# Performance work log

Hardware: AMD Instinct MI355X
Metric: run time of the kernel (lower is better)

The kernel has to match this reference:

```python
import jax, jax.numpy as jnp
import numpy as np

N_HEADS, DK, DV, G = 12, 64, 64, 1
W_WIN, R_RAND = 3, 2
B, S, D = 2, 2048, 768


def _make_idx_tensor(seq_len, g, w, r, seed=0):
    # Mirrors SparseMultiHeadAttention.create_idx_tensor: each middle row is
    # [0] + r random key indices + w consecutive window key indices.
    rng = np.random.default_rng(seed)
    s2 = seq_len - 2 * g
    shift = max(g - (w - 1) // 2, 0)
    windows = np.arange(s2)[:, None] + np.arange(w)[None, :] + shift  # (s2, w)
    rand = np.empty((s2, r), np.int64)
    half = (w - 1) // 2
    for i in range(s2):
        pos = i + g
        cand = rng.choice(np.arange(1, seq_len), size=r + w + 2, replace=False)
        cand = cand[np.abs(cand - pos) > half][:r]
        rand[i] = cand
    idx = np.concatenate([np.zeros((s2, 1), np.int64), rand, windows], axis=1)
    return jnp.asarray(idx)  # (s2, 1+r+w)


def setup_inputs() -> dict:
    key = jax.random.key(0)
    ks = jax.random.split(key, 7)
    scale = 0.02  # keep projected logits in a sane range for softmax
    return {
        "Q": jax.random.normal(ks[0], (B, S, D), jnp.float32),
        "K": jax.random.normal(ks[1], (B, S, D), jnp.float32),
        "V": jax.random.normal(ks[2], (B, S, D), jnp.float32),
        "Wq": jax.random.normal(ks[3], (N_HEADS * DK, D), jnp.float32) * scale,
        "Wk": jax.random.normal(ks[4], (N_HEADS * DK, D), jnp.float32) * scale,
        "Wv": jax.random.normal(ks[5], (N_HEADS * DV, D), jnp.float32) * scale,
        "Wo": jax.random.normal(ks[6], (D, N_HEADS * DV), jnp.float32) * scale,
        "idx_tensor": _make_idx_tensor(S, G, W_WIN, R_RAND),
    }


def reference(Q, K, V, Wq, Wk, Wv, Wo, idx_tensor):
    b, s, d = Q.shape
    h, dk, dv, g = N_HEADS, DK, DV, G
    # projections (torch Linear: x @ W.T), split heads -> (b, h, s, d_head)
    q = (Q @ Wq.T).reshape(b, s, h, dk).transpose(0, 2, 1, 3)
    k = (K @ Wk.T).reshape(b, s, h, dk).transpose(0, 2, 1, 3)
    v = (V @ Wv.T).reshape(b, s, h, dv).transpose(0, 2, 1, 3)

    # global rows (first g, last g) attend densely over all keys
    gidx = jnp.concatenate([jnp.arange(g), jnp.arange(s - g, s)])
    global_attn = jnp.einsum('bhgd,bhtd->bhgt', q[:, :, gidx, :], k)  # (b,h,2g,s)

    # middle rows: gather [first, random..., window...] keys per row
    comb = k[:, :, idx_tensor, :]                    # (b, h, s2, 1+r+w, dk)
    scores = jnp.einsum('bhsd,bhskd->bhsk', q[:, :, g:s - g, :], comb)

    # scatter into a dense (s, s) score matrix (zeros elsewhere), as the source does
    result = jnp.zeros((b, h, s, s), q.dtype)
    result = result.at[:, :, gidx, :].set(global_attn)
    rows = jnp.arange(g, s - g)[:, None]             # (s2, 1)
    result = result.at[:, :, rows, idx_tensor].set(scores)
    result = result / jnp.sqrt(jnp.asarray(dk, q.dtype))

    attn = jax.nn.softmax(result, axis=-1)
    out = jnp.einsum('bhst,bhtd->bhsd', attn, v)     # (b, h, s, dv)
    out = out.transpose(0, 2, 1, 3).reshape(b, s, h * dv)
    return out @ Wo.T
```

## Files before the change

### kernel.cpp

```cpp
#include <hip/hip_runtime.h>
#include <hip/hip_bf16.h>

#define S_LEN   2048
#define D_MODEL 768
#define NH      12
#define HD      64
#define NI      6
#define S2      2046
#define BB      2
#define NCH     8
#define CHK     256

typedef unsigned short ushort_t;
typedef __attribute__((ext_vector_type(8))) short short8v;
typedef __attribute__((ext_vector_type(4))) float f32x4;

__device__ __forceinline__ unsigned short bf16_rne(float x) {
    union { float f; unsigned int u; } c; c.f = x;
    unsigned int u = c.u + 0x7fffu + ((c.u >> 16) & 1u);
    return (unsigned short)(u >> 16);
}
__device__ __forceinline__ float bf16_f(unsigned short h) {
    union { unsigned int u; float f; } c; c.u = ((unsigned int)h) << 16;
    return c.f;
}

__device__ __forceinline__ void gload16(const ushort_t* g, ushort_t* l) {
    __builtin_amdgcn_global_load_lds(
        (const __attribute__((address_space(1))) void*)g,
        (__attribute__((address_space(3))) void*)l, 16, 0, 0);
}

struct CvtAll {
    const float* Q; const float* K; const float* V;
    const float* Wq; const float* Wk; const float* Wv; const float* Wo;
    ushort_t* Qc; ushort_t* Kc; ushort_t* Vc;
    ushort_t* Wqc; ushort_t* Wkc; ushort_t* Wvc; ushort_t* Woc;
    float* vs;
};

__global__ __launch_bounds__(256) void cvt_all(CvtAll a) {
    const int z = blockIdx.z;
    const int tid = threadIdx.x;
    if (z == 4) {
        if (blockIdx.x == 0)
            for (int i = tid; i < BB * D_MODEL; i += 256) a.vs[i] = 0.f;
        return;
    }
    const float* s; ushort_t* d; long i;
    if (z < 3) {
        s = (z == 0) ? a.Q : (z == 1) ? a.K : a.V;
        d = (z == 0) ? a.Qc : (z == 1) ? a.Kc : a.Vc;
        i = ((long)blockIdx.x * 256 + tid) * 8;
    } else {
        const long WSZ = (long)D_MODEL * D_MODEL;
        long f = ((long)blockIdx.x * 256 + tid) * 8;
        if (f >= 4 * WSZ) return;
        const int which = (int)(f / WSZ);
        i = f % WSZ;
        s = (which == 0) ? a.Wq : (which == 1) ? a.Wk : (which == 2) ? a.Wv : a.Wo;
        d = (which == 0) ? a.Wqc : (which == 1) ? a.Wkc : (which == 2) ? a.Wvc : a.Woc;
    }
    float4 v0 = *(const float4*)&s[i];
    float4 v1 = *(const float4*)&s[i + 4];
    short8v o;
    o[0] = (short)bf16_rne(v0.x); o[1] = (short)bf16_rne(v0.y);
    o[2] = (short)bf16_rne(v0.z); o[3] = (short)bf16_rne(v0.w);
    o[4] = (short)bf16_rne(v1.x); o[5] = (short)bf16_rne(v1.y);
    o[6] = (short)bf16_rne(v1.z); o[7] = (short)bf16_rne(v1.w);
    *(short8v*)&d[i] = o;
}

struct GemmArgs { const ushort_t* A; const ushort_t* W; ushort_t* C; float* Cf; float* vs; };

constexpr int GK = 768, GN = 768, GBK = 32, GNT = GK / GBK;

__global__ __launch_bounds__(256) void bf16_gemm_nt(GemmArgs g0, GemmArgs g1, GemmArgs g2) {
    GemmArgs g = (blockIdx.z == 0) ? g0 : ((blockIdx.z == 1) ? g1 : g2);

    __shared__ ushort_t As[3][4096];
    __shared__ ushort_t Bs[3][4096];

    const int tid  = threadIdx.x;
    const int lane = tid & 63;
    const int w    = tid >> 6;
    const int wm   = w & 1;
    const int wn   = w >> 1;
    const int bm   = blockIdx.y * 128;
    const int bn   = blockIdx.x * 128;
    const int fr   = lane & 15;
    const int blkr = lane >> 4;

    f32x4 acc[4][4];
    #pragma unroll
    for (int i = 0; i < 4; ++i)
        #pragma unroll
        for (int j = 0; j < 4; ++j)
            acc[i][j] = (f32x4){0.f, 0.f, 0.f, 0.f};

    const int row0 = tid >> 2;
    const int row1 = row0 + 64;
    const int blk0 = (tid & 3) ^ ((row0 >> 1) & 3);
    const int blk1 = (tid & 3) ^ ((row1 >> 1) & 3);
    const ushort_t* Ag0 = g.A + (size_t)(bm + row0) * GK + blk0 * 8;
    const ushort_t* Ag1 = g.A + (size_t)(bm + row1) * GK + blk1 * 8;
    const ushort_t* Bg0 = g.W + (size_t)(bn + row0) * GK + blk0 * 8;
    const ushort_t* Bg1 = g.W + (size_t)(bn + row1) * GK + blk1 * 8;
    const int l0 = w * 512;
    const int l1 = 2048 + w * 512;

    int aoff[4], boff[4];
    #pragma unroll
    for (int i = 0; i < 4; ++i) {
        const int ra = wm * 64 + i * 16 + fr;
        aoff[i] = (ra * 4 + (blkr ^ ((ra >> 1) & 3))) * 8;
        const int rb = wn * 64 + i * 16 + fr;
        boff[i] = (rb * 4 + (blkr ^ ((rb >> 1) & 3))) * 8;
    }

    gload16(Ag0, &As[0][l0]); gload16(Ag1, &As[0][l1]);
    gload16(Bg0, &Bs[0][l0]); gload16(Bg1, &Bs[0][l1]);
    gload16(Ag0 + GBK, &As[1][l0]); gload16(Ag1 + GBK, &As[1][l1]);
    gload16(Bg0 + GBK, &Bs[1][l0]); gload16(Bg1 + GBK, &Bs[1][l1]);

    for (int t = 0; t < GNT; ++t) {
        if (t < GNT - 1) asm volatile("s_waitcnt vmcnt(4)" ::: "memory");
        else             asm volatile("s_waitcnt vmcnt(0)" ::: "memory");
        __builtin_amdgcn_s_barrier();

        if (t + 2 < GNT) {
            const int ko = (t + 2) * GBK;
            const int nb = (t + 2) % 3;
            gload16(Ag0 + ko, &As[nb][l0]); gload16(Ag1 + ko, &As[nb][l1]);
            gload16(Bg0 + ko, &Bs[nb][l0]); gload16(Bg1 + ko, &Bs[nb][l1]);
        }

        const ushort_t* as = As[t % 3];
        const ushort_t* bs = Bs[t % 3];
        short8v a[4], b[4];
        #pragma unroll
        for (int i = 0; i < 4; ++i) a[i] = *(const short8v*)&as[aoff[i]];
        #pragma unroll
        for (int i = 0; i < 4; ++i) b[i] = *(const short8v*)&bs[boff[i]];
        #pragma unroll
        for (int i = 0; i < 4; ++i)
            #pragma unroll
            for (int j = 0; j < 4; ++j)
                acc[i][j] = __builtin_amdgcn_mfma_f32_16x16x32_bf16(a[i], b[j], acc[i][j], 0, 0, 0);
    }

    const int crow0 = bm + wm * 64 + ((lane >> 4) << 2);
    const int ccol0 = bn + wn * 64 + fr;
    if (g.Cf) {
        #pragma unroll
        for (int i = 0; i < 4; ++i)
            #pragma unroll
            for (int j = 0; j < 4; ++j)
                #pragma unroll
                for (int r = 0; r < 4; ++r)
                    g.Cf[(size_t)(crow0 + i * 16 + r) * GN + ccol0 + j * 16] = acc[i][j][r];
    } else {
        #pragma unroll
        for (int i = 0; i < 4; ++i)
            #pragma unroll
            for (int j = 0; j < 4; ++j)
                #pragma unroll
                for (int r = 0; r < 4; ++r)
                    g.C[(size_t)(crow0 + i * 16 + r) * GN + ccol0 + j * 16] = bf16_rne(acc[i][j][r]);
        if (g.vs) {
            const int bsel = (bm >= S_LEN) ? 1 : 0;
            #pragma unroll
            for (int j = 0; j < 4; ++j) {
                float part = 0.f;
                #pragma unroll
                for (int i = 0; i < 4; ++i)
                    #pragma unroll
                    for (int r = 0; r < 4; ++r)
                        part += bf16_f(bf16_rne(acc[i][j][r]));
                atomicAdd(&g.vs[bsel * D_MODEL + ccol0 + j * 16], part);
            }
        }
    }
}

__global__ __launch_bounds__(768) void sparse_attn(
    const ushort_t* __restrict__ q, const ushort_t* __restrict__ k, const ushort_t* __restrict__ v,
    const float* __restrict__ vsum, const int* __restrict__ idx,
    ushort_t* __restrict__ ao) {
    const int i0 = blockIdx.x * 2;
    const int b = blockIdx.y;
    const int c = threadIdx.x;

    int id[2][NI];
    #pragma unroll
    for (int r = 0; r < 2; ++r)
        #pragma unroll
        for (int j = 0; j < NI; ++j) id[r][j] = idx[(i0 + r) * NI + j];
    bool dup[2][NI];
    #pragma unroll
    for (int r = 0; r < 2; ++r)
        #pragma unroll
        for (int j = 0; j < NI; ++j) {
            bool d = false;
            #pragma unroll
            for (int j2 = 0; j2 < NI; ++j2)
                if (j2 < j) d = d || (id[r][j2] == id[r][j]);
            dup[r][j] = d;
        }

    const size_t rb0 = ((size_t)(b * S_LEN + i0 + 1)) * D_MODEL + c;
    const float qv0 = bf16_f(q[rb0]);
    const float qv1 = bf16_f(q[rb0 + D_MODEL]);

    float kv[2][NI], vv[2][NI];
    #pragma unroll
    for (int r = 0; r < 2; ++r)
        #pragma unroll
        for (int j = 0; j < NI; ++j) {
            const size_t kb = ((size_t)(b * S_LEN + id[r][j])) * D_MODEL + c;
            kv[r][j] = bf16_f(k[kb]);
            vv[r][j] = bf16_f(v[kb]);
        }

    float p[2][NI];
    #pragma unroll
    for (int j = 0; j < NI; ++j) { p[0][j] = qv0 * kv[0][j]; p[1][j] = qv1 * kv[1][j]; }

    #pragma unroll
    for (int off = 32; off; off >>= 1) {
        #pragma unroll
        for (int r = 0; r < 2; ++r)
            #pragma unroll
            for (int j = 0; j < NI; ++j) p[r][j] += __shfl_xor(p[r][j], off);
    }

    const float vsc = vsum[b * D_MODEL + c];
    #pragma unroll
    for (int r = 0; r < 2; ++r) {
        float acc = vsc;
        float Z = 0.f;
        int u = 0;
        #pragma unroll
        for (int j = 0; j < NI; ++j) {
            if (dup[r][j]) continue;
            float e = expf(p[r][j] * 0.125f);
            Z += e;
            u += 1;
            acc += (e - 1.f) * vv[r][j];
        }
        Z += (float)(S_LEN - u);
        ao[rb0 + (size_t)r * D_MODEL] = bf16_rne(acc / Z);
    }
}

__global__ __launch_bounds__(256) void global_attn_part(
    const ushort_t* __restrict__ q, const ushort_t* __restrict__ k, const ushort_t* __restrict__ v,
    float* __restrict__ part) {
    const int ch = blockIdx.x;
    const int rowsel = blockIdx.y;
    const int row = rowsel ? (S_LEN - 1) : 0;
    const int hb = blockIdx.z;
    const int h = hb % NH;
    const int b = hb / NH;
    const int tid = threadIdx.x;

    __shared__ float qs[HD];
    __shared__ float ps[CHK];
    __shared__ float red[8];
    __shared__ float redv[32][72];

    if (tid < HD) qs[tid] = bf16_f(q[((size_t)(b * S_LEN + row)) * D_MODEL + h * HD + tid]);
    __syncthreads();

    const int t = ch * CHK + tid;
    const ushort_t* kp = &k[((size_t)(b * S_LEN + t)) * D_MODEL + h * HD];
    float s = 0.f;
    #pragma unroll
    for (int dd = 0; dd < 8; ++dd) {
        short8v kk = *(const short8v*)&kp[dd * 8];
        #pragma unroll
        for (int e = 0; e < 8; ++e)
            s += qs[dd * 8 + e] * bf16_f((unsigned short)kk[e]);
    }
    s *= 0.125f;

    float m = s;
    #pragma unroll
    for (int off = 32; off; off >>= 1) m = fmaxf(m, __shfl_xor(m, off));
    if ((tid & 63) == 0) red[tid >> 6] = m;
    __syncthreads();
    m = fmaxf(fmaxf(red[0], red[1]), fmaxf(red[2], red[3]));

    float e = expf(s - m);
    ps[tid] = e;
    float zp = e;
    #pragma unroll
    for (int off = 32; off; off >>= 1) zp += __shfl_xor(zp, off);
    if ((tid & 63) == 0) red[4 + (tid >> 6)] = zp;
    __syncthreads();
    const float E = red[4] + red[5] + red[6] + red[7];

    const int g8 = tid >> 3;
    const int d8 = (tid & 7) * 8;
    float a8[8] = {};
    for (int tt = g8; tt < CHK; tt += 32) {
        const float wgt = ps[tt];
        short8v v8 = *(const short8v*)&v[((size_t)(b * S_LEN + ch * CHK + tt)) * D_MODEL + h * HD + d8];
        #pragma unroll
        for (int e2 = 0; e2 < 8; ++e2)
            a8[e2] += wgt * bf16_f((unsigned short)v8[e2]);
    }
    #pragma unroll
    for (int e2 = 0; e2 < 8; ++e2) redv[g8][d8 + e2] = a8[e2];
    __syncthreads();
    if (tid < HD) {
        float o = 0.f;
        #pragma unroll
        for (int gg = 0; gg < 32; ++gg) o += redv[gg][tid];
        float* pr = part + ((size_t)((hb * 2 + rowsel) * NCH + ch)) * (HD + 2);
        pr[2 + tid] = o;
        if (tid == 0) { pr[0] = m; pr[1] = E; }
    }
}

__global__ __launch_bounds__(64) void global_attn_fin(
    const float* __restrict__ part, ushort_t* __restrict__ ao) {
    const int rb = blockIdx.x;
    const int rowsel = rb & 1;
    const int hb = rb >> 1;
    const int h = hb % NH;
    const int b = hb / NH;
    const int row = rowsel ? (S_LEN - 1) : 0;
    const int d = threadIdx.x;

    const float* pr = part + (size_t)rb * NCH * (HD + 2);
    float M = -1e30f;
    #pragma unroll
    for (int c = 0; c < NCH; ++c) M = fmaxf(M, pr[c * (HD + 2)]);
    float Z = 0.f, acc = 0.f;
    #pragma unroll
    for (int c = 0; c < NCH; ++c) {
        float wgt = expf(pr[c * (HD + 2)] - M);
        Z   += pr[c * (HD + 2) + 1] * wgt;
        acc += pr[c * (HD + 2) + 2 + d] * wgt;
    }
    ao[((size_t)(b * S_LEN + row)) * D_MODEL + h * HD + d] = bf16_rne(acc / Z);
}

extern "C" void kernel_launch(void* const* d_in, const int* in_sizes, int n_in,
                              void* d_out, int out_size, void* d_ws, size_t ws_size,
                              hipStream_t stream) {
    const float* Q  = (const float*)d_in[0];
    const float* K  = (const float*)d_in[1];
    const float* V  = (const float*)d_in[2];
    const float* Wq = (const float*)d_in[3];
    const float* Wk = (const float*)d_in[4];
    const float* Wv = (const float*)d_in[5];
    const float* Wo = (const float*)d_in[6];
    const int*  idx = (const int*)d_in[7];
    float* out = (float*)d_out;

    const size_t SZ  = (size_t)BB * S_LEN * D_MODEL;
    const size_t WSZ = (size_t)D_MODEL * D_MODEL;

    ushort_t* Qc  = (ushort_t*)d_ws;
    ushort_t* Kc  = Qc  + SZ;
    ushort_t* Vc  = Kc  + SZ;
    ushort_t* Wqc = Vc  + SZ;
    ushort_t* Wkc = Wqc + WSZ;
    ushort_t* Wvc = Wkc + WSZ;
    ushort_t* Woc = Wvc + WSZ;
    ushort_t* qb  = Woc + WSZ;
    ushort_t* kb  = qb  + SZ;
    ushort_t* vb  = kb  + SZ;
    ushort_t* ao  = vb  + SZ;
    float* vs   = (float*)(ao + SZ);
    float* part = vs + BB * D_MODEL;

    {
        CvtAll a{Q, K, V, Wq, Wk, Wv, Wo, Qc, Kc, Vc, Wqc, Wkc, Wvc, Woc, vs};
        cvt_all<<<dim3((unsigned)(SZ / 2048), 1, 5), 256, 0, stream>>>(a);
    }
    {
        GemmArgs g0{Qc, Wqc, qb, nullptr, nullptr};
        GemmArgs g1{Kc, Wkc, kb, nullptr, nullptr};
        GemmArgs g2{Vc, Wvc, vb, nullptr, vs};
        bf16_gemm_nt<<<dim3(D_MODEL / 128, BB * S_LEN / 128, 3), 256, 0, stream>>>(g0, g1, g2);
    }
    sparse_attn<<<dim3(S2 / 2, BB), 768, 0, stream>>>(qb, kb, vb, vs, idx, ao);
    global_attn_part<<<dim3(NCH, 2, NH * BB), 256, 0, stream>>>(qb, kb, vb, part);
    global_attn_fin<<<dim3(2 * NH * BB), 64, 0, stream>>>(part, ao);
    {
        GemmArgs g{ao, Woc, nullptr, out, nullptr};
        bf16_gemm_nt<<<dim3(D_MODEL / 128, BB * S_LEN / 128, 1), 256, 0, stream>>>(g, g, g);
    }
}
```

Before: 198.2 us.

## Shrink GEMM M-tile to 64, deepen prefetch to 4 stages, remap workgroups

The bf16 NT GEMM tile shrinks from 128x128 to 64x128, which doubles the workgroup count: 1152 for the QKV projection and 384 for the output projection. This is meant to fill more of the GPU's compute units. The shared-memory pipeline goes from 3 to 4 buffers with a prefetch distance of 3, and the waitcnt thresholds are adjusted to match. Workgroup IDs are remapped with a stride-8 interleave so that neighbouring blocks are spread out across groups. In exchange, each block reuses less data per MFMA and reloads the weight tiles more often.

```diff
diff --git a/kernel.cpp b/kernel.cpp
--- a/kernel.cpp
+++ b/kernel.cpp
@@ -74,86 +74,99 @@
 struct GemmArgs { const ushort_t* A; const ushort_t* W; ushort_t* C; float* Cf; float* vs; };
 
 constexpr int GK = 768, GN = 768, GBK = 32, GNT = GK / GBK;
+constexpr int GX = 6, GY = 64;
 
 __global__ __launch_bounds__(256) void bf16_gemm_nt(GemmArgs g0, GemmArgs g1, GemmArgs g2) {
-    GemmArgs g = (blockIdx.z == 0) ? g0 : ((blockIdx.z == 1) ? g1 : g2);
-
-    __shared__ ushort_t As[3][4096];
-    __shared__ ushort_t Bs[3][4096];
+    const int nwg = GX * GY * gridDim.z;
+    int flat = (blockIdx.z * GY + blockIdx.y) * GX + blockIdx.x;
+    flat = (flat & 7) * (nwg >> 3) + (flat >> 3);
+    const int bz = flat / (GX * GY);
+    const int rem = flat - bz * (GX * GY);
+    const int by = rem / GX;
+    const int bx = rem - by * GX;
+
+    GemmArgs g = (bz == 0) ? g0 : ((bz == 1) ? g1 : g2);
+
+    __shared__ ushort_t As[4][2048];
+    __shared__ ushort_t Bs[4][4096];
 
     const int tid  = threadIdx.x;
     const int lane = tid & 63;
     const int w    = tid >> 6;
     const int wm   = w & 1;
     const int wn   = w >> 1;
-    const int bm   = blockIdx.y * 128;
-    const int bn   = blockIdx.x * 128;
+    const int bm   = by * 64;
+    const int bn   = bx * 128;
     const int fr   = lane & 15;
     const int blkr = lane >> 4;
 
-    f32x4 acc[4][4];
-    #pragma unroll
-    for (int i = 0; i < 4; ++i)
+    f32x4 acc[2][4];
+    #pragma unroll
+    for (int i = 0; i < 2; ++i)
         #pragma unroll
         for (int j = 0; j < 4; ++j)
             acc[i][j] = (f32x4){0.f, 0.f, 0.f, 0.f};
 
     const int row0 = tid >> 2;
-    const int row1 = row0 + 64;
     const int blk0 = (tid & 3) ^ ((row0 >> 1) & 3);
-    const int blk1 = (tid & 3) ^ ((row1 >> 1) & 3);
-    const ushort_t* Ag0 = g.A + (size_t)(bm + row0) * GK + blk0 * 8;
-    const ushort_t* Ag1 = g.A + (size_t)(bm + row1) * GK + blk1 * 8;
+    const ushort_t* Ag  = g.A + (size_t)(bm + row0) * GK + blk0 * 8;
     const ushort_t* Bg0 = g.W + (size_t)(bn + row0) * GK + blk0 * 8;
-    const ushort_t* Bg1 = g.W + (size_t)(bn + row1) * GK + blk1 * 8;
+    const ushort_t* Bg1 = g.W + (size_t)(bn + row0 + 64) * GK + blk0 * 8;
     const int l0 = w * 512;
-    const int l1 = 2048 + w * 512;
-
-    int aoff[4], boff[4];
-    #pragma unroll
-    for (int i = 0; i < 4; ++i) {
-        const int ra = wm * 64 + i * 16 + fr;
+
+    int aoff[2], boff[4];
+    #pragma unroll
+    for (int i = 0; i < 2; ++i) {
+        const int ra = wm * 32 + i * 16 + fr;
         aoff[i] = (ra * 4 + (blkr ^ ((ra >> 1) & 3))) * 8;
-        const int rb = wn * 64 + i * 16 + fr;
-        boff[i] = (rb * 4 + (blkr ^ ((rb >> 1) & 3))) * 8;
-    }
-
-    gload16(Ag0, &As[0][l0]); gload16(Ag1, &As[0][l1]);
-    gload16(Bg0, &Bs[0][l0]); gload16(Bg1, &Bs[0][l1]);
-    gload16(Ag0 + GBK, &As[1][l0]); gload16(Ag1 + GBK, &As[1][l1]);
-    gload16(Bg0 + GBK, &Bs[1][l0]); gload16(Bg1 + GBK, &Bs[1][l1]);
+    }
+    #pragma unroll
+    for (int j = 0; j < 4; ++j) {
+        const int rb = wn * 64 + j * 16 + fr;
+        boff[j] = (rb * 4 + (blkr ^ ((rb >> 1) & 3))) * 8;
+    }
+
+    #pragma unroll
+    for (int t = 0; t < 3; ++t) {
+        const int ko = t * GBK;
+        gload16(Ag + ko, &As[t][l0]);
+        gload16(Bg0 + ko, &Bs[t][l0]);
+        gload16(Bg1 + ko, &Bs[t][2048 + l0]);
+    }
 
     for (int t = 0; t < GNT; ++t) {
-        if (t < GNT - 1) asm volatile("s_waitcnt vmcnt(4)" ::: "memory");
-        else             asm volatile("s_waitcnt vmcnt(0)" ::: "memory");
+        if (t < GNT - 2)      asm volatile("s_waitcnt vmcnt(6)" ::: "memory");
+        else if (t == GNT - 2) asm volatile("s_waitcnt vmcnt(3)" ::: "memory");
+        else                  asm volatile("s_waitcnt vmcnt(0)" ::: "memory");
         __builtin_amdgcn_s_barrier();
 
-        if (t + 2 < GNT) {
-            const int ko = (t + 2) * GBK;
-            const int nb = (t + 2) % 3;
-            gload16(Ag0 + ko, &As[nb][l0]); gload16(Ag1 + ko, &As[nb][l1]);
-            gload16(Bg0 + ko, &Bs[nb][l0]); gload16(Bg1 + ko, &Bs[nb][l1]);
+        if (t + 3 < GNT) {
+            const int ko = (t + 3) * GBK;
+            const int nb = (t + 3) & 3;
+            gload16(Ag + ko, &As[nb][l0]);
+            gload16(Bg0 + ko, &Bs[nb][l0]);
+            gload16(Bg1 + ko, &Bs[nb][2048 + l0]);
         }
 
-        const ushort_t* as = As[t % 3];
-        const ushort_t* bs = Bs[t % 3];
-        short8v a[4], b[4];
-        #pragma unroll
-        for (int i = 0; i < 4; ++i) a[i] = *(const short8v*)&as[aoff[i]];
-        #pragma unroll
-        for (int i = 0; i < 4; ++i) b[i] = *(const short8v*)&bs[boff[i]];
-        #pragma unroll
-        for (int i = 0; i < 4; ++i)
+        const ushort_t* as = As[t & 3];
+        const ushort_t* bs = Bs[t & 3];
+        short8v a[2], b[4];
+        #pragma unroll
+        for (int i = 0; i < 2; ++i) a[i] = *(const short8v*)&as[aoff[i]];
+        #pragma unroll
+        for (int j = 0; j < 4; ++j) b[j] = *(const short8v*)&bs[boff[j]];
+        #pragma unroll
+        for (int i = 0; i < 2; ++i)
             #pragma unroll
             for (int j = 0; j < 4; ++j)
                 acc[i][j] = __builtin_amdgcn_mfma_f32_16x16x32_bf16(a[i], b[j], acc[i][j], 0, 0, 0);
     }
 
-    const int crow0 = bm + wm * 64 + ((lane >> 4) << 2);
+    const int crow0 = bm + wm * 32 + ((lane >> 4) << 2);
     const int ccol0 = bn + wn * 64 + fr;
     if (g.Cf) {
         #pragma unroll
-        for (int i = 0; i < 4; ++i)
+        for (int i = 0; i < 2; ++i)
             #pragma unroll
             for (int j = 0; j < 4; ++j)
                 #pragma unroll
@@ -161,7 +174,7 @@
                     g.Cf[(size_t)(crow0 + i * 16 + r) * GN + ccol0 + j * 16] = acc[i][j][r];
     } else {
         #pragma unroll
-        for (int i = 0; i < 4; ++i)
+        for (int i = 0; i < 2; ++i)
             #pragma unroll
             for (int j = 0; j < 4; ++j)
                 #pragma unroll
@@ -173,7 +186,7 @@
             for (int j = 0; j < 4; ++j) {
                 float part = 0.f;
                 #pragma unroll
-                for (int i = 0; i < 4; ++i)
+                for (int i = 0; i < 2; ++i)
                     #pragma unroll
                     for (int r = 0; r < 4; ++r)
                         part += bf16_f(bf16_rne(acc[i][j][r]));
@@ -385,13 +398,13 @@
         GemmArgs g0{Qc, Wqc, qb, nullptr, nullptr};
         GemmArgs g1{Kc, Wkc, kb, nullptr, nullptr};
         GemmArgs g2{Vc, Wvc, vb, nullptr, vs};
-        bf16_gemm_nt<<<dim3(D_MODEL / 128, BB * S_LEN / 128, 3), 256, 0, stream>>>(g0, g1, g2);
+        bf16_gemm_nt<<<dim3(GX, GY, 3), 256, 0, stream>>>(g0, g1, g2);
     }
     sparse_attn<<<dim3(S2 / 2, BB), 768, 0, stream>>>(qb, kb, vb, vs, idx, ao);
     global_attn_part<<<dim3(NCH, 2, NH * BB), 256, 0, stream>>>(qb, kb, vb, part);
     global_attn_fin<<<dim3(2 * NH * BB), 64, 0, stream>>>(part, ao);
     {
         GemmArgs g{ao, Woc, nullptr, out, nullptr};
-        bf16_gemm_nt<<<dim3(D_MODEL / 128, BB * S_LEN / 128, 1), 256, 0, stream>>>(g, g, g);
-    }
-}
+        bf16_gemm_nt<<<dim3(GX, GY, 1), 256, 0, stream>>>(g, g, g);
+    }
+}
```

Result: slower. 206.3 us (+4.1%).

## Fuse sparse and global attention kernels and remap GEMM workgroups across XCDs

Applied to the files above, without the earlier changes.

Merges the sparse-row attention kernel and the global-row partial attention kernel into one launch, with block ranges dispatched by block index. The global part now runs with 768 threads and spreads its V accumulation over 96 groups. The GEMM also remaps flat workgroup IDs with an XCD-style stride-8 swizzle so neighbouring tiles land on the same chiplet for better L2 reuse. This removes one launch and lets both attention pieces overlap, at the cost of a larger shared-memory footprint per block and more idle threads in the global branch.

```diff
diff --git a/kernel.cpp b/kernel.cpp
--- a/kernel.cpp
+++ b/kernel.cpp
@@ -10,6 +10,7 @@
 #define BB      2
 #define NCH     8
 #define CHK     256
+#define SPB     (S2 / 2)
 
 typedef unsigned short ushort_t;
 typedef __attribute__((ext_vector_type(8))) short short8v;
@@ -74,9 +75,18 @@
 struct GemmArgs { const ushort_t* A; const ushort_t* W; ushort_t* C; float* Cf; float* vs; };
 
 constexpr int GK = 768, GN = 768, GBK = 32, GNT = GK / GBK;
+constexpr int GX = 6, GY = 32;
 
 __global__ __launch_bounds__(256) void bf16_gemm_nt(GemmArgs g0, GemmArgs g1, GemmArgs g2) {
-    GemmArgs g = (blockIdx.z == 0) ? g0 : ((blockIdx.z == 1) ? g1 : g2);
+    const int nwg = GX * GY * gridDim.z;
+    int flat = (blockIdx.z * GY + blockIdx.y) * GX + blockIdx.x;
+    flat = (flat & 7) * (nwg >> 3) + (flat >> 3);
+    const int bz = flat / (GX * GY);
+    const int rem = flat - bz * (GX * GY);
+    const int by = rem / GX;
+    const int bx = rem - by * GX;
+
+    GemmArgs g = (bz == 0) ? g0 : ((bz == 1) ? g1 : g2);
 
     __shared__ ushort_t As[3][4096];
     __shared__ ushort_t Bs[3][4096];
@@ -86,8 +96,8 @@
     const int w    = tid >> 6;
     const int wm   = w & 1;
     const int wn   = w >> 1;
-    const int bm   = blockIdx.y * 128;
-    const int bn   = blockIdx.x * 128;
+    const int bm   = by * 128;
+    const int bn   = bx * 128;
     const int fr   = lane & 15;
     const int blkr = lane >> 4;
 
@@ -183,127 +193,131 @@
     }
 }
 
-__global__ __launch_bounds__(768) void sparse_attn(
+__global__ __launch_bounds__(768) void attn_fused(
     const ushort_t* __restrict__ q, const ushort_t* __restrict__ k, const ushort_t* __restrict__ v,
     const float* __restrict__ vsum, const int* __restrict__ idx,
-    ushort_t* __restrict__ ao) {
-    const int i0 = blockIdx.x * 2;
-    const int b = blockIdx.y;
-    const int c = threadIdx.x;
-
-    int id[2][NI];
-    #pragma unroll
-    for (int r = 0; r < 2; ++r)
-        #pragma unroll
-        for (int j = 0; j < NI; ++j) id[r][j] = idx[(i0 + r) * NI + j];
-    bool dup[2][NI];
-    #pragma unroll
-    for (int r = 0; r < 2; ++r)
-        #pragma unroll
-        for (int j = 0; j < NI; ++j) {
-            bool d = false;
-            #pragma unroll
-            for (int j2 = 0; j2 < NI; ++j2)
-                if (j2 < j) d = d || (id[r][j2] == id[r][j]);
-            dup[r][j] = d;
-        }
-
-    const size_t rb0 = ((size_t)(b * S_LEN + i0 + 1)) * D_MODEL + c;
-    const float qv0 = bf16_f(q[rb0]);
-    const float qv1 = bf16_f(q[rb0 + D_MODEL]);
-
-    float kv[2][NI], vv[2][NI];
-    #pragma unroll
-    for (int r = 0; r < 2; ++r)
-        #pragma unroll
-        for (int j = 0; j < NI; ++j) {
-            const size_t kb = ((size_t)(b * S_LEN + id[r][j])) * D_MODEL + c;
-            kv[r][j] = bf16_f(k[kb]);
-            vv[r][j] = bf16_f(v[kb]);
-        }
-
-    float p[2][NI];
-    #pragma unroll
-    for (int j = 0; j < NI; ++j) { p[0][j] = qv0 * kv[0][j]; p[1][j] = qv1 * kv[1][j]; }
-
-    #pragma unroll
-    for (int off = 32; off; off >>= 1) {
-        #pragma unroll
-        for (int r = 0; r < 2; ++r)
-            #pragma unroll
-            for (int j = 0; j < NI; ++j) p[r][j] += __shfl_xor(p[r][j], off);
-    }
-
-    const float vsc = vsum[b * D_MODEL + c];
-    #pragma unroll
-    for (int r = 0; r < 2; ++r) {
-        float acc = vsc;
-        float Z = 0.f;
-        int u = 0;
-        #pragma unroll
-        for (int j = 0; j < NI; ++j) {
-            if (dup[r][j]) continue;
-            float e = expf(p[r][j] * 0.125f);
-            Z += e;
-            u += 1;
-            acc += (e - 1.f) * vv[r][j];
-        }
-        Z += (float)(S_LEN - u);
-        ao[rb0 + (size_t)r * D_MODEL] = bf16_rne(acc / Z);
-    }
-}
-
-__global__ __launch_bounds__(256) void global_attn_part(
-    const ushort_t* __restrict__ q, const ushort_t* __restrict__ k, const ushort_t* __restrict__ v,
-    float* __restrict__ part) {
-    const int ch = blockIdx.x;
-    const int rowsel = blockIdx.y;
-    const int row = rowsel ? (S_LEN - 1) : 0;
-    const int hb = blockIdx.z;
-    const int h = hb % NH;
-    const int b = hb / NH;
+    float* __restrict__ part, ushort_t* __restrict__ ao) {
+    const int bid = blockIdx.x;
     const int tid = threadIdx.x;
 
     __shared__ float qs[HD];
     __shared__ float ps[CHK];
     __shared__ float red[8];
-    __shared__ float redv[32][72];
+    __shared__ float redv[96][72];
+
+    if (bid < SPB * BB) {
+        const int b = bid & 1;
+        const int i0 = (bid >> 1) * 2;
+        const int c = tid;
+
+        int id[2][NI];
+        #pragma unroll
+        for (int r = 0; r < 2; ++r)
+            #pragma unroll
+            for (int j = 0; j < NI; ++j) id[r][j] = idx[(i0 + r) * NI + j];
+        bool dup[2][NI];
+        #pragma unroll
+        for (int r = 0; r < 2; ++r)
+            #pragma unroll
+            for (int j = 0; j < NI; ++j) {
+                bool d = false;
+                #pragma unroll
+                for (int j2 = 0; j2 < NI; ++j2)
+                    if (j2 < j) d = d || (id[r][j2] == id[r][j]);
+                dup[r][j] = d;
+            }
+
+        const size_t rb0 = ((size_t)(b * S_LEN + i0 + 1)) * D_MODEL + c;
+        const float qv0 = bf16_f(q[rb0]);
+        const float qv1 = bf16_f(q[rb0 + D_MODEL]);
+
+        float kv[2][NI], vv[2][NI];
+        #pragma unroll
+        for (int r = 0; r < 2; ++r)
+            #pragma unroll
+            for (int j = 0; j < NI; ++j) {
+                const size_t kb = ((size_t)(b * S_LEN + id[r][j])) * D_MODEL + c;
+                kv[r][j] = bf16_f(k[kb]);
+                vv[r][j] = bf16_f(v[kb]);
+            }
+
+        float p[2][NI];
+        #pragma unroll
+        for (int j = 0; j < NI; ++j) { p[0][j] = qv0 * kv[0][j]; p[1][j] = qv1 * kv[1][j]; }
+
+        #pragma unroll
+        for (int off = 32; off; off >>= 1) {
+            #pragma unroll
+            for (int r = 0; r < 2; ++r)
+                #pragma unroll
+                for (int j = 0; j < NI; ++j) p[r][j] += __shfl_xor(p[r][j], off);
+        }
+
+        const float vsc = vsum[b * D_MODEL + c];
+        #pragma unroll
+        for (int r = 0; r < 2; ++r) {
+            float acc = vsc;
+            float Z = 0.f;
+            int u = 0;
+            #pragma unroll
+            for (int j = 0; j < NI; ++j) {
+                if (dup[r][j]) continue;
+                float e = expf(p[r][j] * 0.125f);
+                Z += e;
+                u += 1;
+                acc += (e - 1.f) * vv[r][j];
+            }
+            Z += (float)(S_LEN - u);
+            ao[rb0 + (size_t)r * D_MODEL] = bf16_rne(acc / Z);
+        }
+        return;
+    }
+
+    const int pid = bid - SPB * BB;
+    const int ch = pid & 7;
+    const int rowsel = (pid >> 3) & 1;
+    const int hb = pid >> 4;
+    const int h = hb % NH;
+    const int b = hb / NH;
+    const int row = rowsel ? (S_LEN - 1) : 0;
 
     if (tid < HD) qs[tid] = bf16_f(q[((size_t)(b * S_LEN + row)) * D_MODEL + h * HD + tid]);
     __syncthreads();
 
-    const int t = ch * CHK + tid;
-    const ushort_t* kp = &k[((size_t)(b * S_LEN + t)) * D_MODEL + h * HD];
     float s = 0.f;
-    #pragma unroll
-    for (int dd = 0; dd < 8; ++dd) {
-        short8v kk = *(const short8v*)&kp[dd * 8];
-        #pragma unroll
-        for (int e = 0; e < 8; ++e)
-            s += qs[dd * 8 + e] * bf16_f((unsigned short)kk[e]);
-    }
-    s *= 0.125f;
+    if (tid < CHK) {
+        const int t = ch * CHK + tid;
+        const ushort_t* kp = &k[((size_t)(b * S_LEN + t)) * D_MODEL + h * HD];
+        #pragma unroll
+        for (int dd = 0; dd < 8; ++dd) {
+            short8v kk = *(const short8v*)&kp[dd * 8];
+            #pragma unroll
+            for (int e = 0; e < 8; ++e)
+                s += qs[dd * 8 + e] * bf16_f((unsigned short)kk[e]);
+        }
+        s *= 0.125f;
+    }
 
     float m = s;
     #pragma unroll
     for (int off = 32; off; off >>= 1) m = fmaxf(m, __shfl_xor(m, off));
-    if ((tid & 63) == 0) red[tid >> 6] = m;
+    if (tid < CHK && (tid & 63) == 0) red[tid >> 6] = m;
     __syncthreads();
     m = fmaxf(fmaxf(red[0], red[1]), fmaxf(red[2], red[3]));
 
-    float e = expf(s - m);
-    ps[tid] = e;
+    float e = (tid < CHK) ? expf(s - m) : 0.f;
+    if (tid < CHK) ps[tid] = e;
     float zp = e;
     #pragma unroll
     for (int off = 32; off; off >>= 1) zp += __shfl_xor(zp, off);
-    if ((tid & 63) == 0) red[4 + (tid >> 6)] = zp;
+    if (tid < CHK && (tid & 63) == 0) red[4 + (tid >> 6)] = zp;
     __syncthreads();
     const float E = red[4] + red[5] + red[6] + red[7];
 
     const int g8 = tid >> 3;
     const int d8 = (tid & 7) * 8;
     float a8[8] = {};
-    for (int tt = g8; tt < CHK; tt += 32) {
+    for (int tt = g8; tt < CHK; tt += 96) {
         const float wgt = ps[tt];
         short8v v8 = *(const short8v*)&v[((size_t)(b * S_LEN + ch * CHK + tt)) * D_MODEL + h * HD + d8];
         #pragma unroll
@@ -316,7 +330,7 @@
     if (tid < HD) {
         float o = 0.f;
         #pragma unroll
-        for (int gg = 0; gg < 32; ++gg) o += redv[gg][tid];
+        for (int gg = 0; gg < 96; ++gg) o += redv[gg][tid];
         float* pr = part + ((size_t)((hb * 2 + rowsel) * NCH + ch)) * (HD + 2);
         pr[2 + tid] = o;
         if (tid == 0) { pr[0] = m; pr[1] = E; }
@@ -385,13 +399,13 @@
         GemmArgs g0{Qc, Wqc, qb, nullptr, nullptr};
         GemmArgs g1{Kc, Wkc, kb, nullptr, nullptr};
         GemmArgs g2{Vc, Wvc, vb, nullptr, vs};
-        bf16_gemm_nt<<<dim3(D_MODEL / 128, BB * S_LEN / 128, 3), 256, 0, stream>>>(g0, g1, g2);
-    }
-    sparse_attn<<<dim3(S2 / 2, BB), 768, 0, stream>>>(qb, kb, vb, vs, idx, ao);
-    global_attn_part<<<dim3(NCH, 2, NH * BB), 256, 0, stream>>>(qb, kb, vb, part);
+        bf16_gemm_nt<<<dim3(GX, GY, 3), 256, 0, stream>>>(g0, g1, g2);
+    }
+    attn_fused<<<dim3(SPB * BB + NCH * 2 * NH * BB), 768, 0, stream>>>(
+        qb, kb, vb, vs, idx, part, ao);
     global_attn_fin<<<dim3(2 * NH * BB), 64, 0, stream>>>(part, ao);
     {
         GemmArgs g{ao, Woc, nullptr, out, nullptr};
-        bf16_gemm_nt<<<dim3(D_MODEL / 128, BB * S_LEN / 128, 1), 256, 0, stream>>>(g, g, g);
-    }
-}
+        bf16_gemm_nt<<<dim3(GX, GY, 1), 256, 0, stream>>>(g, g, g);
+    }
+}
```

New measurement: 192.6 us. -2.8%, faster.
